# Performance work log

Hardware: AMD Instinct MI355X
Metric: run time of the kernel (lower is better)

## Reference

```python
import jax, jax.numpy as jnp
import numpy as np

D_MODEL = 1024
NUM_HEADS = 16
D_K = D_MODEL // NUM_HEADS


def setup_inputs() -> dict:
    key = jax.random.key(0)
    ks = jax.random.split(key, 11)
    B, S = 2, 2048
    scale = 1.0 / np.sqrt(D_MODEL)
    inp = {
        'q': jax.random.normal(ks[0], (B, S, D_MODEL), dtype=jnp.float32),
        'k': jax.random.normal(ks[1], (B, S, D_MODEL), dtype=jnp.float32),
        'v': jax.random.normal(ks[2], (B, S, D_MODEL), dtype=jnp.float32),
        'W_q': jax.random.normal(ks[3], (D_MODEL, D_MODEL), dtype=jnp.float32) * scale,
        'b_q': jnp.zeros((D_MODEL,), dtype=jnp.float32),
        'W_k': jax.random.normal(ks[4], (D_MODEL, D_MODEL), dtype=jnp.float32) * scale,
        'b_k': jnp.zeros((D_MODEL,), dtype=jnp.float32),
        'W_v': jax.random.normal(ks[5], (D_MODEL, D_MODEL), dtype=jnp.float32) * scale,
        'b_v': jnp.zeros((D_MODEL,), dtype=jnp.float32),
        'W_o': jax.random.normal(ks[6], (D_MODEL, D_MODEL), dtype=jnp.float32) * scale,
        'b_o': jnp.zeros((D_MODEL,), dtype=jnp.float32),
    }
    return inp


def _split_heads(x):
    # [B, S, D] -> [B, H, S, d_k]
    B, S, _ = x.shape
    return x.reshape(B, S, NUM_HEADS, D_K).transpose(0, 2, 1, 3)


def reference(q, k, v, W_q, b_q, W_k, b_k, W_v, b_v, W_o, b_o):
    # Linear projections (torch Linear: x @ W.T + b)
    qh = _split_heads(q @ W_q.T + b_q)  # [B,H,S,dk]
    kh = _split_heads(k @ W_k.T + b_k)
    vh = _split_heads(v @ W_v.T + b_v)
    scores = jnp.einsum('bhsd,bhtd->bhst', qh, kh) / jnp.sqrt(
        jnp.asarray(D_K, dtype=qh.dtype))  # [B,H,S,S]
    probs = jax.nn.softmax(scores, axis=-1)
    attn = jnp.einsum('bhst,bhtd->bhsd', probs, vh)  # [B,H,S,dk]
    B, H, S, dk = attn.shape
    combined = attn.transpose(0, 2, 1, 3).reshape(B, S, H * dk)  # [B,S,D]
    return combined @ W_o.T + b_o
```

## Files before the change

### kernel.cpp

```cpp
#include <hip/hip_runtime.h>
#include <hip/hip_bf16.h>

typedef __bf16 bf16;
typedef __attribute__((ext_vector_type(4))) __bf16 bf16x4;
typedef __attribute__((ext_vector_type(8))) __bf16 bf16x8;
typedef __attribute__((ext_vector_type(4))) float f32x4;
typedef __attribute__((ext_vector_type(4))) short short4v;

#define AS1C(p) ((const __attribute__((address_space(1))) void*)(p))
#define AS3(p)  ((__attribute__((address_space(3))) void*)(p))

static constexpr int B_ = 2, S_ = 2048, DM = 1024, H_ = 16, DK = 64;
static constexpr int M_ = B_ * S_;
static constexpr int NW = DM * DM;
static constexpr float QSCL = 0.125f * 1.44269504088896340736f;

__device__ __forceinline__ float fast_exp2(float x) {
#if __has_builtin(__builtin_amdgcn_exp2f)
  return __builtin_amdgcn_exp2f(x);
#else
  return exp2f(x);
#endif
}

__device__ __forceinline__ f32x4 mfma_pv(bf16x4 a, bf16x4 b, f32x4 c) {
#if __has_builtin(__builtin_amdgcn_mfma_f32_16x16x16_bf16)
  return __builtin_amdgcn_mfma_f32_16x16x16_bf16(a, b, c, 0, 0, 0);
#else
  union U { bf16x4 h; short4v s; };
  U ua; ua.h = a;
  U ub; ub.h = b;
  return __builtin_amdgcn_mfma_f32_16x16x16bf16_1k(ua.s, ub.s, c, 0, 0, 0);
#endif
}

__global__ __launch_bounds__(256) void cast_w4(
    const float* Wq, const float* Wk, const float* Wv, const float* Wo,
    bf16* Wc, bf16* WoC)
{
  const int z = blockIdx.y;
  const float* in = z == 0 ? Wq : (z == 1 ? Wk : (z == 2 ? Wv : Wo));
  const float s = z == 0 ? QSCL : 1.0f;
  bf16* out = z < 3 ? (Wc + (size_t)z * NW) : WoC;
  const int i = (blockIdx.x * 256 + threadIdx.x) * 8;
  f32x4 a = *(const f32x4*)(in + i);
  f32x4 b = *(const f32x4*)(in + i + 4);
  bf16x8 o;
#pragma unroll
  for (int j = 0; j < 4; ++j) { o[j] = (bf16)(a[j] * s); o[4 + j] = (bf16)(b[j] * s); }
  *(bf16x8*)(out + i) = o;
}

__global__ __launch_bounds__(256) void gemm_qkv(
    const float* A0, const float* A1, const float* A2,
    const bf16* __restrict__ Wc,
    const float* b0, const float* b1, const float* b2,
    bf16* C0, bf16* C1, bf16* C2, int M, int N, int K)
{
  const int id = blockIdx.x;
  const int z  = id >> 8;
  const int r  = id & 255;
  const int by = r & 31;
  const int bx = r >> 5;
  const float* A = z == 0 ? A0 : (z == 1 ? A1 : A2);
  const float* bias = z == 0 ? b0 : (z == 1 ? b1 : b2);
  const float bscale = z == 0 ? QSCL : 1.0f;
  const bf16* W = Wc + (size_t)z * NW;
  bf16* Cout = z == 0 ? C0 : (z == 1 ? C1 : C2);
  const bool transv = (z == 2);

  __shared__ bf16 As[2 * 128 * 32];
  __shared__ bf16 Bs[2 * 128 * 32];

  const int tid  = threadIdx.x;
  const int wave = tid >> 6, lane = tid & 63;
  const int quad = lane >> 4, l16 = lane & 15;
  const int wm = wave >> 1, wn = wave & 1;
  const int row0 = by * 128;
  const int col0 = bx * 128;

  const int srow  = lane >> 2;
  const int skcol = (lane & 3) * 8;

  const int arow  = (tid >> 1) & 127;
  const int ak16  = (tid & 1) * 16;
  const float* agp = A + (size_t)(row0 + arow) * K + ak16;
  f32x4 pre[8];
#pragma unroll
  for (int hf = 0; hf < 2; ++hf)
#pragma unroll
    for (int c = 0; c < 4; ++c)
      pre[hf * 4 + c] = *(const f32x4*)(agp + hf * 32 + c * 4);

  f32x4 acc[4][4] = {};

  for (int k0 = 0; k0 < K; k0 += 64) {
    __syncthreads();
#pragma unroll
    for (int hf = 0; hf < 2; ++hf) {
      bf16x8 w0, w1;
#pragma unroll
      for (int j = 0; j < 4; ++j) {
        w0[j]     = (bf16)pre[hf * 4 + 0][j];
        w0[4 + j] = (bf16)pre[hf * 4 + 1][j];
        w1[j]     = (bf16)pre[hf * 4 + 2][j];
        w1[4 + j] = (bf16)pre[hf * 4 + 3][j];
      }
      bf16* dst = As + hf * 4096 + arow * 32 + ak16;
      *(bf16x8*)dst = w0;
      *(bf16x8*)(dst + 8) = w1;
    }
#pragma unroll
    for (int hf = 0; hf < 2; ++hf)
#pragma unroll
      for (int i = 0; i < 2; ++i) {
        const int c = wave * 2 + i;
        __builtin_amdgcn_global_load_lds(
            AS1C(W + (size_t)(col0 + c * 16 + srow) * K + k0 + hf * 32 + skcol),
            AS3(Bs + hf * 4096 + c * 512), 16, 0, 0);
      }
    __syncthreads();

    if (k0 + 64 < K) {
#pragma unroll
      for (int hf = 0; hf < 2; ++hf)
#pragma unroll
        for (int c = 0; c < 4; ++c)
          pre[hf * 4 + c] = *(const f32x4*)(agp + k0 + 64 + hf * 32 + c * 4);
    }

#pragma unroll
    for (int hf = 0; hf < 2; ++hf) {
      bf16x8 a[4], bfr[4];
#pragma unroll
      for (int i = 0; i < 4; ++i)
        a[i] = *(const bf16x8*)(As + hf * 4096 + (wm * 64 + i * 16 + l16) * 32 + quad * 8);
#pragma unroll
      for (int j = 0; j < 4; ++j)
        bfr[j] = *(const bf16x8*)(Bs + hf * 4096 + (wn * 64 + j * 16 + l16) * 32 + quad * 8);
#pragma unroll
      for (int i = 0; i < 4; ++i)
#pragma unroll
        for (int j = 0; j < 4; ++j)
          acc[i][j] = __builtin_amdgcn_mfma_f32_16x16x32_bf16(a[i], bfr[j], acc[i][j], 0, 0, 0);
    }
  }

#pragma unroll
  for (int j = 0; j < 4; ++j) {
    const int col = col0 + wn * 64 + j * 16 + l16;
    const float bv = bias[col] * bscale;
    if (transv) {
      const int hh = col >> 6, dd = col & 63;
#pragma unroll
      for (int i = 0; i < 4; ++i) {
        const int row = row0 + wm * 64 + i * 16 + quad * 4;
        const int bb2 = row >> 11, tok = row & 2047;
        bf16x4 o;
#pragma unroll
        for (int r = 0; r < 4; ++r) o[r] = (bf16)(acc[i][j][r] + bv);
        *(bf16x4*)(Cout + (((size_t)bb2 * H_ + hh) * DK + dd) * S_ + tok) = o;
      }
    } else {
#pragma unroll
      for (int i = 0; i < 4; ++i)
#pragma unroll
        for (int r = 0; r < 4; ++r) {
          const int row = row0 + wm * 64 + i * 16 + quad * 4 + r;
          Cout[(size_t)row * N + col] = (bf16)(acc[i][j][r] + bv);
        }
    }
  }
}

__global__ __launch_bounds__(256, 2) void gemm_out(
    const bf16* __restrict__ Ain, const bf16* __restrict__ W,
    const float* __restrict__ bias, float* __restrict__ Cout,
    int M, int N, int K)
{
  const int id = blockIdx.x;
  const int by = id & 63;
  const int bx = id >> 6;

  __shared__ bf16 As0[2 * 64 * 32], As1[2 * 64 * 32];
  __shared__ bf16 Bs0[2 * 128 * 32], Bs1[2 * 128 * 32];

  const int tid  = threadIdx.x;
  const int wave = tid >> 6, lane = tid & 63;
  const int quad = lane >> 4, l16 = lane & 15;
  const int wm = wave >> 1, wn = wave & 1;
  const int row0 = by * 64;
  const int col0 = bx * 128;

  const int srow  = lane >> 2;
  const int skcol = (lane & 3) * 8;

  auto stage_A = [&](int k0, bf16* dst) {
#pragma unroll
    for (int hf = 0; hf < 2; ++hf)
      __builtin_amdgcn_global_load_lds(
          AS1C(Ain + (size_t)(row0 + wave * 16 + srow) * K + k0 + hf * 32 + skcol),
          AS3(dst + hf * 2048 + wave * 512), 16, 0, 0);
  };
  auto stage_W = [&](int k0, bf16* dst) {
#pragma unroll
    for (int hf = 0; hf < 2; ++hf)
#pragma unroll
      for (int i = 0; i < 2; ++i) {
        const int c = wave * 2 + i;
        __builtin_amdgcn_global_load_lds(
            AS1C(W + (size_t)(col0 + c * 16 + srow) * K + k0 + hf * 32 + skcol),
            AS3(dst + hf * 4096 + c * 512), 16, 0, 0);
      }
  };

  f32x4 acc[2][4] = {};

  auto mfma_tile = [&](const bf16* Ab, const bf16* Bb) {
#pragma unroll
    for (int hf = 0; hf < 2; ++hf) {
      bf16x8 a[2], bfr[4];
#pragma unroll
      for (int i = 0; i < 2; ++i)
        a[i] = *(const bf16x8*)(Ab + hf * 2048 + (wm * 32 + i * 16 + l16) * 32 + quad * 8);
#pragma unroll
      for (int j = 0; j < 4; ++j)
        bfr[j] = *(const bf16x8*)(Bb + hf * 4096 + (wn * 64 + j * 16 + l16) * 32 + quad * 8);
#pragma unroll
      for (int i = 0; i < 2; ++i)
#pragma unroll
        for (int j = 0; j < 4; ++j)
          acc[i][j] = __builtin_amdgcn_mfma_f32_16x16x32_bf16(a[i], bfr[j], acc[i][j], 0, 0, 0);
    }
  };

  const int NK = K / 64;
  stage_A(0, As0);
  stage_W(0, Bs0);
  __syncthreads();

  for (int t2 = 0; t2 < NK / 2; ++t2) {
    const int t = t2 * 2;
    if (t + 1 < NK) { stage_A((t + 1) * 64, As1); stage_W((t + 1) * 64, Bs1); }
    mfma_tile(As0, Bs0);
    __syncthreads();
    if (t + 2 < NK) { stage_A((t + 2) * 64, As0); stage_W((t + 2) * 64, Bs0); }
    mfma_tile(As1, Bs1);
    __syncthreads();
  }

#pragma unroll
  for (int j = 0; j < 4; ++j) {
    const int col = col0 + wn * 64 + j * 16 + l16;
    const float bv = bias[col];
#pragma unroll
    for (int i = 0; i < 2; ++i)
#pragma unroll
      for (int r = 0; r < 4; ++r) {
        const int row = row0 + wm * 32 + i * 16 + quad * 4 + r;
        Cout[(size_t)row * N + col] = acc[i][j][r] + bv;
      }
  }
}

__global__ __launch_bounds__(256, 2) void attn_kernel(
    const bf16* Q, const bf16* __restrict__ Kb,
    const bf16* __restrict__ Vtg, bf16* O)
{
  __shared__ bf16 Kt[2 * 64 * 64];
  __shared__ bf16 Vt[2 * 64 * 64];

  const int tid  = threadIdx.x;
  const int wave = tid >> 6, lane = tid & 63;
  const int quad = lane >> 4, l16 = lane & 15;
  const int id = blockIdx.x;
  const int hb = id & 31;
  const int h = hb & 15, b = hb >> 4;
  const int qt = id >> 5;
  const int qA = qt * 128 + wave * 32;
  const size_t base  = (size_t)b * S_ * DM + (size_t)h * DK;
  const size_t baseV = ((size_t)b * H_ + h) * DK * S_;

  bf16x8 qf[2][2];
#pragma unroll
  for (int f = 0; f < 2; ++f)
#pragma unroll
    for (int kt = 0; kt < 2; ++kt)
      qf[f][kt] = *(const bf16x8*)(Q + base + (size_t)(qA + f * 16 + l16) * DM + kt * 32 + quad * 8);

  const bool kside = (wave < 2);
  const int srow  = kside ? (tid >> 1) : ((tid - 128) >> 1);
  const int shalf = tid & 1;
  const bf16* gp = kside
      ? (Kb + base + (size_t)srow * DM + shalf * 32)
      : (Vtg + baseV + (size_t)srow * S_ + shalf * 32);
  const size_t gstep = kside ? (size_t)64 * DM : 64;
  char* sb = (char*)(kside ? (void*)Kt : (void*)Vt) + srow * 128;
  const int sw_s = (srow & 7) << 4;

  bf16x8 st[4];
#pragma unroll
  for (int c = 0; c < 4; ++c) st[c] = *(const bf16x8*)(gp + c * 8);
  gp += gstep;
#pragma unroll
  for (int c = 0; c < 4; ++c)
    *(bf16x8*)(sb + ((shalf * 64 + c * 16) ^ sw_s)) = st[c];
#pragma unroll
  for (int c = 0; c < 4; ++c) st[c] = *(const bf16x8*)(gp + c * 8);
  gp += gstep;

  f32x4 lacc[2] = {};
  f32x4 accO[2][4] = {};
  const int sw = (l16 & 7) << 4;

  __syncthreads();

  constexpr int NIT = S_ / 64;
  for (int it = 0; it < NIT; ++it) {
    const int cur = it & 1, nxt = cur ^ 1;
    const char* Kc = (const char*)Kt + cur * 8192;
    const char* Vc = (const char*)Vt + cur * 8192;

    f32x4 sc[2][4];
#pragma unroll
    for (int ct = 0; ct < 4; ++ct) {
      const char* kp = Kc + (ct * 16 + l16) * 128;
      const bf16x8 kf0 = *(const bf16x8*)(kp + ((quad * 16) ^ sw));
      const bf16x8 kf1 = *(const bf16x8*)(kp + ((64 + quad * 16) ^ sw));
#pragma unroll
      for (int f = 0; f < 2; ++f) {
        f32x4 a = {0.f, 0.f, 0.f, 0.f};
        a = __builtin_amdgcn_mfma_f32_16x16x32_bf16(kf0, qf[f][0], a, 0, 0, 0);
        a = __builtin_amdgcn_mfma_f32_16x16x32_bf16(kf1, qf[f][1], a, 0, 0, 0);
        sc[f][ct] = a;
      }
    }

    if (it + 1 < NIT) {
#pragma unroll
      for (int c = 0; c < 4; ++c)
        *(bf16x8*)(sb + nxt * 8192 + ((shalf * 64 + c * 16) ^ sw_s)) = st[c];
      if (it + 2 < NIT) {
#pragma unroll
        for (int c = 0; c < 4; ++c) st[c] = *(const bf16x8*)(gp + c * 8);
        gp += gstep;
      }
    }

    bf16x4 pk[2][4];
#pragma unroll
    for (int f = 0; f < 2; ++f)
#pragma unroll
      for (int ct = 0; ct < 4; ++ct)
#pragma unroll
        for (int r = 0; r < 4; ++r) {
          const float p = fast_exp2(sc[f][ct][r]);
          lacc[f][r] += p;
          pk[f][ct][r] = (bf16)p;
        }

#pragma unroll
    for (int dt = 0; dt < 4; ++dt) {
      const char* vp = Vc + (dt * 16 + l16) * 128;
#pragma unroll
      for (int ct = 0; ct < 4; ++ct) {
        const bf16x4 vf = *(const bf16x4*)(vp + ((ct * 32 + quad * 8) ^ sw));
#pragma unroll
        for (int f = 0; f < 2; ++f)
          accO[f][dt] = mfma_pv(vf, pk[f][ct], accO[f][dt]);
      }
    }

    __syncthreads();
  }

#pragma unroll
  for (int f = 0; f < 2; ++f) {
    float l_s = (lacc[f][0] + lacc[f][1]) + (lacc[f][2] + lacc[f][3]);
    l_s += __shfl_xor(l_s, 16, 64);
    l_s += __shfl_xor(l_s, 32, 64);
    const float inv = 1.0f / l_s;
#pragma unroll
    for (int dt = 0; dt < 4; ++dt) {
      bf16x4 o;
#pragma unroll
      for (int r = 0; r < 4; ++r) o[r] = (bf16)(accO[f][dt][r] * inv);
      *(bf16x4*)(O + base + (size_t)(qA + f * 16 + l16) * DM + dt * 16 + quad * 4) = o;
    }
  }
}

extern "C" void kernel_launch(void* const* d_in, const int* in_sizes, int n_in,
                              void* d_out, int out_size, void* d_ws, size_t ws_size,
                              hipStream_t stream) {
  (void)in_sizes; (void)n_in; (void)out_size; (void)ws_size;
  const float* q  = (const float*)d_in[0];
  const float* k  = (const float*)d_in[1];
  const float* v  = (const float*)d_in[2];
  const float* Wq = (const float*)d_in[3];
  const float* bq = (const float*)d_in[4];
  const float* Wk = (const float*)d_in[5];
  const float* bk = (const float*)d_in[6];
  const float* Wv = (const float*)d_in[7];
  const float* bvv= (const float*)d_in[8];
  const float* Wo = (const float*)d_in[9];
  const float* bo = (const float*)d_in[10];
  float* out = (float*)d_out;

  char* ws = (char*)d_ws;
  const size_t MB = 1024 * 1024;
  bf16* Qb  = (bf16*)(ws);
  bf16* Kbf = (bf16*)(ws + 8 * MB);
  bf16* Vtg = (bf16*)(ws + 16 * MB);
  bf16* Wc  = (bf16*)(ws + 24 * MB);
  bf16* WoC = (bf16*)(ws + 30 * MB);
  bf16* Ab  = Qb;

  dim3 bb(256, 1, 1);

  cast_w4<<<dim3(NW / 2048, 4, 1), bb, 0, stream>>>(Wq, Wk, Wv, Wo, Wc, WoC);

  gemm_qkv<<<dim3(768, 1, 1), bb, 0, stream>>>(
      q, k, v, Wc, bq, bk, bvv, Qb, Kbf, Vtg, M_, DM, DM);

  attn_kernel<<<dim3(512, 1, 1), bb, 0, stream>>>(Qb, Kbf, Vtg, Ab);

  gemm_out<<<dim3(512, 1, 1), bb, 0, stream>>>(Ab, WoC, bo, out, M_, DM, DM);
}
```

Baseline: 217.0 us.

## Double-buffer A tile in QKV GEMM and load W fragments directly to registers

The QKV projection GEMM now ping-pongs between two LDS buffers for the converted A tile and prefetches A two steps ahead, leaving one barrier per k-step instead of two. The weight operand skips LDS and is read straight from global memory into MFMA register fragments, and launch bounds request 3 blocks per SM. This targets barrier stalls and LDS staging of W, but relies on L2 reuse for the weight rows, adds register pressure from the extra fragments and prefetch registers, and hardcodes K=1024 through NK=16.

Result: slower. 240.9 us (+11.0%).

```diff
diff --git a/kernel.cpp b/kernel.cpp
--- a/kernel.cpp
+++ b/kernel.cpp
@@ -51,7 +51,7 @@
   *(bf16x8*)(out + i) = o;
 }
 
-__global__ __launch_bounds__(256) void gemm_qkv(
+__global__ __launch_bounds__(256, 3) void gemm_qkv(
     const float* A0, const float* A1, const float* A2,
     const bf16* __restrict__ Wc,
     const float* b0, const float* b1, const float* b2,
@@ -69,8 +69,8 @@
   bf16* Cout = z == 0 ? C0 : (z == 1 ? C1 : C2);
   const bool transv = (z == 2);
 
-  __shared__ bf16 As[2 * 128 * 32];
-  __shared__ bf16 Bs[2 * 128 * 32];
+  __shared__ bf16 As0[2 * 128 * 32];
+  __shared__ bf16 As1[2 * 128 * 32];
 
   const int tid  = threadIdx.x;
   const int wave = tid >> 6, lane = tid & 63;
@@ -79,23 +79,21 @@
   const int row0 = by * 128;
   const int col0 = bx * 128;
 
-  const int srow  = lane >> 2;
-  const int skcol = (lane & 3) * 8;
-
   const int arow  = (tid >> 1) & 127;
   const int ak16  = (tid & 1) * 16;
   const float* agp = A + (size_t)(row0 + arow) * K + ak16;
+
+  const bf16* wbase = W + (size_t)(col0 + wn * 64 + l16) * K + quad * 8;
+
   f32x4 pre[8];
-#pragma unroll
-  for (int hf = 0; hf < 2; ++hf)
-#pragma unroll
-    for (int c = 0; c < 4; ++c)
-      pre[hf * 4 + c] = *(const f32x4*)(agp + hf * 32 + c * 4);
-
-  f32x4 acc[4][4] = {};
-
-  for (int k0 = 0; k0 < K; k0 += 64) {
-    __syncthreads();
+  auto loadA = [&](int t) {
+#pragma unroll
+    for (int hf = 0; hf < 2; ++hf)
+#pragma unroll
+      for (int c = 0; c < 4; ++c)
+        pre[hf * 4 + c] = *(const f32x4*)(agp + t * 64 + hf * 32 + c * 4);
+  };
+  auto cvtwrite = [&](bf16* An) {
 #pragma unroll
     for (int hf = 0; hf < 2; ++hf) {
       bf16x8 w0, w1;
@@ -106,44 +104,49 @@
         w1[j]     = (bf16)pre[hf * 4 + 2][j];
         w1[4 + j] = (bf16)pre[hf * 4 + 3][j];
       }
-      bf16* dst = As + hf * 4096 + arow * 32 + ak16;
+      bf16* dst = An + hf * 4096 + arow * 32 + ak16;
       *(bf16x8*)dst = w0;
       *(bf16x8*)(dst + 8) = w1;
     }
+  };
+
+  f32x4 acc[4][4] = {};
+  constexpr int NK = 16;
+
+  auto step = [&](int t, const bf16* Ac, bf16* An) {
+    bf16x8 wf[2][4];
 #pragma unroll
     for (int hf = 0; hf < 2; ++hf)
 #pragma unroll
-      for (int i = 0; i < 2; ++i) {
-        const int c = wave * 2 + i;
-        __builtin_amdgcn_global_load_lds(
-            AS1C(W + (size_t)(col0 + c * 16 + srow) * K + k0 + hf * 32 + skcol),
-            AS3(Bs + hf * 4096 + c * 512), 16, 0, 0);
-      }
+      for (int j = 0; j < 4; ++j)
+        wf[hf][j] = *(const bf16x8*)(wbase + (size_t)j * 16 * K + t * 64 + hf * 32);
+
+    if (t + 1 < NK) cvtwrite(An);
+    if (t + 2 < NK) loadA(t + 2);
+
+#pragma unroll
+    for (int hf = 0; hf < 2; ++hf) {
+      bf16x8 a[4];
+#pragma unroll
+      for (int i = 0; i < 4; ++i)
+        a[i] = *(const bf16x8*)(Ac + hf * 4096 + (wm * 64 + i * 16 + l16) * 32 + quad * 8);
+#pragma unroll
+      for (int i = 0; i < 4; ++i)
+#pragma unroll
+        for (int j = 0; j < 4; ++j)
+          acc[i][j] = __builtin_amdgcn_mfma_f32_16x16x32_bf16(a[i], wf[hf][j], acc[i][j], 0, 0, 0);
+    }
     __syncthreads();
-
-    if (k0 + 64 < K) {
-#pragma unroll
-      for (int hf = 0; hf < 2; ++hf)
-#pragma unroll
-        for (int c = 0; c < 4; ++c)
-          pre[hf * 4 + c] = *(const f32x4*)(agp + k0 + 64 + hf * 32 + c * 4);
-    }
-
-#pragma unroll
-    for (int hf = 0; hf < 2; ++hf) {
-      bf16x8 a[4], bfr[4];
-#pragma unroll
-      for (int i = 0; i < 4; ++i)
-        a[i] = *(const bf16x8*)(As + hf * 4096 + (wm * 64 + i * 16 + l16) * 32 + quad * 8);
-#pragma unroll
-      for (int j = 0; j < 4; ++j)
-        bfr[j] = *(const bf16x8*)(Bs + hf * 4096 + (wn * 64 + j * 16 + l16) * 32 + quad * 8);
-#pragma unroll
-      for (int i = 0; i < 4; ++i)
-#pragma unroll
-        for (int j = 0; j < 4; ++j)
-          acc[i][j] = __builtin_amdgcn_mfma_f32_16x16x32_bf16(a[i], bfr[j], acc[i][j], 0, 0, 0);
-    }
+  };
+
+  loadA(0);
+  cvtwrite(As0);
+  loadA(1);
+  __syncthreads();
+
+  for (int t = 0; t < NK; t += 2) {
+    step(t,     As0, As1);
+    step(t + 1, As1, As0);
   }
 
 #pragma unroll
@@ -158,16 +161,16 @@
         const int bb2 = row >> 11, tok = row & 2047;
         bf16x4 o;
 #pragma unroll
-        for (int r = 0; r < 4; ++r) o[r] = (bf16)(acc[i][j][r] + bv);
+        for (int r2 = 0; r2 < 4; ++r2) o[r2] = (bf16)(acc[i][j][r2] + bv);
         *(bf16x4*)(Cout + (((size_t)bb2 * H_ + hh) * DK + dd) * S_ + tok) = o;
       }
     } else {
 #pragma unroll
       for (int i = 0; i < 4; ++i)
 #pragma unroll
-        for (int r = 0; r < 4; ++r) {
-          const int row = row0 + wm * 64 + i * 16 + quad * 4 + r;
-          Cout[(size_t)row * N + col] = (bf16)(acc[i][j][r] + bv);
+        for (int r2 = 0; r2 < 4; ++r2) {
+          const int row = row0 + wm * 64 + i * 16 + quad * 4 + r2;
+          Cout[(size_t)row * N + col] = (bf16)(acc[i][j][r2] + bv);
         }
     }
   }
```

## Pre-cast q/k/v activations to bf16 and use async LDS-load QKV GEMM

Applied to the files above, without the earlier changes.

Extends the weight cast kernel to also convert the q, k and v activations to bf16 in workspace. When the workspace is large enough, a new QKV GEMM streams the bf16 tiles directly into LDS with global_load_lds and a 64-wide K step, replacing the fp32 load-and-convert path. This is meant to halve the A-operand bytes the GEMM reads and take conversion off its critical path, at the cost of an extra full read and write of the activations in the cast kernel. Whether it runs depends on ws_size being at least 60 MB; otherwise the old fp32 GEMM path is used.

Measured after the change: 209.3 us. 1.04x faster.

```diff
diff --git a/kernel.cpp b/kernel.cpp
--- a/kernel.cpp
+++ b/kernel.cpp
@@ -34,24 +34,135 @@
 #endif
 }
 
-__global__ __launch_bounds__(256) void cast_w4(
+__global__ __launch_bounds__(256) void cast_all(
     const float* Wq, const float* Wk, const float* Wv, const float* Wo,
-    bf16* Wc, bf16* WoC)
+    const float* q, const float* k, const float* v,
+    bf16* Wc, bf16* WoC, bf16* qc, bf16* kc, bf16* vc)
 {
-  const int z = blockIdx.y;
-  const float* in = z == 0 ? Wq : (z == 1 ? Wk : (z == 2 ? Wv : Wo));
-  const float s = z == 0 ? QSCL : 1.0f;
-  bf16* out = z < 3 ? (Wc + (size_t)z * NW) : WoC;
-  const int i = (blockIdx.x * 256 + threadIdx.x) * 8;
+  const int id = blockIdx.x;
+  const float* in;
+  bf16* out;
+  float s = 1.0f;
+  int base;
+  if (id < 2048) {
+    const int z = id >> 9;
+    base = id & 511;
+    in  = z == 0 ? Wq : (z == 1 ? Wk : (z == 2 ? Wv : Wo));
+    out = z < 3 ? (Wc + (size_t)z * NW) : WoC;
+    if (z == 0) s = QSCL;
+  } else {
+    const int z = (id - 2048) >> 11;
+    base = (id - 2048) & 2047;
+    in  = z == 0 ? q : (z == 1 ? k : v);
+    out = z == 0 ? qc : (z == 1 ? kc : vc);
+  }
+  const size_t i = ((size_t)base * 256 + threadIdx.x) * 8;
   f32x4 a = *(const f32x4*)(in + i);
-  f32x4 b = *(const f32x4*)(in + i + 4);
+  f32x4 b2 = *(const f32x4*)(in + i + 4);
   bf16x8 o;
 #pragma unroll
-  for (int j = 0; j < 4; ++j) { o[j] = (bf16)(a[j] * s); o[4 + j] = (bf16)(b[j] * s); }
+  for (int j = 0; j < 4; ++j) { o[j] = (bf16)(a[j] * s); o[4 + j] = (bf16)(b2[j] * s); }
   *(bf16x8*)(out + i) = o;
 }
 
-__global__ __launch_bounds__(256) void gemm_qkv(
+__global__ __launch_bounds__(256, 3) void gemm_qkv_b(
+    const bf16* __restrict__ qc, const bf16* __restrict__ kc,
+    const bf16* __restrict__ vc, const bf16* __restrict__ Wc,
+    const float* b0, const float* b1, const float* b2,
+    bf16* C0, bf16* C1, bf16* C2, int M, int N, int K)
+{
+  const int id = blockIdx.x;
+  const int z  = id >> 8;
+  const int r  = id & 255;
+  const int by = r & 31;
+  const int bx = r >> 5;
+  const bf16* A = z == 0 ? qc : (z == 1 ? kc : vc);
+  const float* bias = z == 0 ? b0 : (z == 1 ? b1 : b2);
+  const float bscale = z == 0 ? QSCL : 1.0f;
+  const bf16* W = Wc + (size_t)z * NW;
+  bf16* Cout = z == 0 ? C0 : (z == 1 ? C1 : C2);
+  const bool transv = (z == 2);
+
+  __shared__ bf16 As[2 * 128 * 32];
+  __shared__ bf16 Bs[2 * 128 * 32];
+
+  const int tid  = threadIdx.x;
+  const int wave = tid >> 6, lane = tid & 63;
+  const int quad = lane >> 4, l16 = lane & 15;
+  const int wm = wave >> 1, wn = wave & 1;
+  const int row0 = by * 128;
+  const int col0 = bx * 128;
+
+  const int srow  = lane >> 2;
+  const int skcol = (lane & 3) * 8;
+
+  f32x4 acc[4][4] = {};
+
+  for (int k0 = 0; k0 < K; k0 += 64) {
+    __syncthreads();
+#pragma unroll
+    for (int hf = 0; hf < 2; ++hf)
+#pragma unroll
+      for (int c = wave; c < 8; c += 4)
+        __builtin_amdgcn_global_load_lds(
+            AS1C(A + (size_t)(row0 + c * 16 + srow) * K + k0 + hf * 32 + skcol),
+            AS3(As + hf * 4096 + c * 512), 16, 0, 0);
+#pragma unroll
+    for (int hf = 0; hf < 2; ++hf)
+#pragma unroll
+      for (int i = 0; i < 2; ++i) {
+        const int c = wave * 2 + i;
+        __builtin_amdgcn_global_load_lds(
+            AS1C(W + (size_t)(col0 + c * 16 + srow) * K + k0 + hf * 32 + skcol),
+            AS3(Bs + hf * 4096 + c * 512), 16, 0, 0);
+      }
+    __syncthreads();
+
+#pragma unroll
+    for (int hf = 0; hf < 2; ++hf) {
+      bf16x8 a[4], bfr[4];
+#pragma unroll
+      for (int i = 0; i < 4; ++i)
+        a[i] = *(const bf16x8*)(As + hf * 4096 + (wm * 64 + i * 16 + l16) * 32 + quad * 8);
+#pragma unroll
+      for (int j = 0; j < 4; ++j)
+        bfr[j] = *(const bf16x8*)(Bs + hf * 4096 + (wn * 64 + j * 16 + l16) * 32 + quad * 8);
+#pragma unroll
+      for (int i = 0; i < 4; ++i)
+#pragma unroll
+        for (int j = 0; j < 4; ++j)
+          acc[i][j] = __builtin_amdgcn_mfma_f32_16x16x32_bf16(a[i], bfr[j], acc[i][j], 0, 0, 0);
+    }
+  }
+
+#pragma unroll
+  for (int j = 0; j < 4; ++j) {
+    const int col = col0 + wn * 64 + j * 16 + l16;
+    const float bv = bias[col] * bscale;
+    if (transv) {
+      const int hh = col >> 6, dd = col & 63;
+#pragma unroll
+      for (int i = 0; i < 4; ++i) {
+        const int row = row0 + wm * 64 + i * 16 + quad * 4;
+        const int bb2 = row >> 11, tok = row & 2047;
+        bf16x4 o;
+#pragma unroll
+        for (int r2 = 0; r2 < 4; ++r2) o[r2] = (bf16)(acc[i][j][r2] + bv);
+        *(bf16x4*)(Cout + (((size_t)bb2 * H_ + hh) * DK + dd) * S_ + tok) = o;
+      }
+    } else {
+#pragma unroll
+      for (int i = 0; i < 4; ++i)
+#pragma unroll
+        for (int r2 = 0; r2 < 4; ++r2) {
+          const int row = row0 + wm * 64 + i * 16 + quad * 4 + r2;
+          Cout[(size_t)row * N + col] = (bf16)(acc[i][j][r2] + bv);
+        }
+    }
+  }
+}
+
+__global__ __launch_bounds__(256) void gemm_qkv_f(
     const float* A0, const float* A1, const float* A2,
     const bf16* __restrict__ Wc,
     const float* b0, const float* b1, const float* b2,
@@ -158,16 +269,16 @@
         const int bb2 = row >> 11, tok = row & 2047;
         bf16x4 o;
 #pragma unroll
-        for (int r = 0; r < 4; ++r) o[r] = (bf16)(acc[i][j][r] + bv);
+        for (int r2 = 0; r2 < 4; ++r2) o[r2] = (bf16)(acc[i][j][r2] + bv);
         *(bf16x4*)(Cout + (((size_t)bb2 * H_ + hh) * DK + dd) * S_ + tok) = o;
       }
     } else {
 #pragma unroll
       for (int i = 0; i < 4; ++i)
 #pragma unroll
-        for (int r = 0; r < 4; ++r) {
-          const int row = row0 + wm * 64 + i * 16 + quad * 4 + r;
-          Cout[(size_t)row * N + col] = (bf16)(acc[i][j][r] + bv);
+        for (int r2 = 0; r2 < 4; ++r2) {
+          const int row = row0 + wm * 64 + i * 16 + quad * 4 + r2;
+          Cout[(size_t)row * N + col] = (bf16)(acc[i][j][r2] + bv);
         }
     }
   }
@@ -393,7 +504,7 @@
 extern "C" void kernel_launch(void* const* d_in, const int* in_sizes, int n_in,
                               void* d_out, int out_size, void* d_ws, size_t ws_size,
                               hipStream_t stream) {
-  (void)in_sizes; (void)n_in; (void)out_size; (void)ws_size;
+  (void)in_sizes; (void)n_in; (void)out_size;
   const float* q  = (const float*)d_in[0];
   const float* k  = (const float*)d_in[1];
   const float* v  = (const float*)d_in[2];
@@ -414,14 +525,24 @@
   bf16* Vtg = (bf16*)(ws + 16 * MB);
   bf16* Wc  = (bf16*)(ws + 24 * MB);
   bf16* WoC = (bf16*)(ws + 30 * MB);
+  bf16* qc  = (bf16*)(ws + 32 * MB);
+  bf16* kc  = (bf16*)(ws + 40 * MB);
+  bf16* vc  = (bf16*)(ws + 48 * MB);
   bf16* Ab  = Qb;
 
+  const bool big = ws_size >= 60 * MB;
   dim3 bb(256, 1, 1);
 
-  cast_w4<<<dim3(NW / 2048, 4, 1), bb, 0, stream>>>(Wq, Wk, Wv, Wo, Wc, WoC);
-
-  gemm_qkv<<<dim3(768, 1, 1), bb, 0, stream>>>(
-      q, k, v, Wc, bq, bk, bvv, Qb, Kbf, Vtg, M_, DM, DM);
+  cast_all<<<dim3(big ? 8192 : 2048, 1, 1), bb, 0, stream>>>(
+      Wq, Wk, Wv, Wo, q, k, v, Wc, WoC, qc, kc, vc);
+
+  if (big) {
+    gemm_qkv_b<<<dim3(768, 1, 1), bb, 0, stream>>>(
+        qc, kc, vc, Wc, bq, bk, bvv, Qb, Kbf, Vtg, M_, DM, DM);
+  } else {
+    gemm_qkv_f<<<dim3(768, 1, 1), bb, 0, stream>>>(
+        q, k, v, Wc, bq, bk, bvv, Qb, Kbf, Vtg, M_, DM, DM);
+  }
 
   attn_kernel<<<dim3(512, 1, 1), bb, 0, stream>>>(Qb, Kbf, Vtg, Ab);
 
```
